# Optimization experiments

Measured on AMD Instinct MI355X. Metric: run time of the kernel, lower is better.

## Reference

```python
import jax, jax.numpy as jnp
import numpy as np

DIM = 512
B = 16
L = 2048
MLP_RATIO = 4
GATE_HID = max(DIM // 4, 8)  # 128
EPS = 1e-5


def _ln(x, g, b):
    mu = jnp.mean(x, axis=-1, keepdims=True)
    var = jnp.mean(jnp.square(x - mu), axis=-1, keepdims=True)
    return (x - mu) * jax.lax.rsqrt(var + EPS) * g + b


def _dwconv(h, w, b, pad):
    # h: [B, C, L], w: [C, 1, k] depthwise
    y = jax.lax.conv_general_dilated(
        h, w, window_strides=(1,), padding=[(pad, pad)],
        dimension_numbers=('NCH', 'OIH', 'NCH'), feature_group_count=h.shape[1])
    return y + b[None, :, None]


def setup_inputs() -> dict:
    key = jax.random.key(0)
    ks = jax.random.split(key, 16)
    d = DIM
    hid = d * MLP_RATIO
    s = lambda k, shape, scale: jax.random.normal(k, shape, dtype=jnp.float32) * scale
    return {
        'x': jax.random.normal(ks[0], (B, L, d), dtype=jnp.float32),
        'ln1_g': jnp.ones((d,), jnp.float32), 'ln1_b': jnp.zeros((d,), jnp.float32),
        'w3': s(ks[1], (d, 1, 3), 0.3), 'b3': jnp.zeros((d,), jnp.float32),
        'w5': s(ks[2], (d, 1, 5), 0.3), 'b5': jnp.zeros((d,), jnp.float32),
        'w7': s(ks[3], (d, 1, 7), 0.3), 'b7': jnp.zeros((d,), jnp.float32),
        'wmix': s(ks[4], (d, d), 0.03), 'bmix': jnp.zeros((d,), jnp.float32),
        'cg_w1': s(ks[5], (d, GATE_HID), 0.03), 'cg_b1': jnp.zeros((GATE_HID,), jnp.float32),
        'cg_w2': s(ks[6], (GATE_HID, d), 0.05), 'cg_b2': jnp.zeros((d,), jnp.float32),
        'wout': s(ks[7], (d, d), 0.03), 'bout': jnp.zeros((d,), jnp.float32),
        'ls1': jnp.full((d,), 1e-4, jnp.float32),
        'ln2_g': jnp.ones((d,), jnp.float32), 'ln2_b': jnp.zeros((d,), jnp.float32),
        'ffn_w1': s(ks[8], (d, hid), 0.03), 'ffn_b1': jnp.zeros((hid,), jnp.float32),
        'ffn_w2': s(ks[9], (hid, d), 0.02), 'ffn_b2': jnp.zeros((d,), jnp.float32),
        'ls2': jnp.full((d,), 1e-4, jnp.float32),
    }


def reference(x, ln1_g, ln1_b, w3, b3, w5, b5, w7, b7, wmix, bmix,
              cg_w1, cg_b1, cg_w2, cg_b2, wout, bout, ls1,
              ln2_g, ln2_b, ffn_w1, ffn_b1, ffn_w2, ffn_b2, ls2):
    gelu = lambda v: jax.nn.gelu(v, approximate=False)
    # norm + transpose to channels-first [B, D, L]
    h = jnp.transpose(_ln(x, ln1_g, ln1_b), (0, 2, 1))
    mixed = (_dwconv(h, w3, b3, 1) + _dwconv(h, w5, b5, 2) + _dwconv(h, w7, b7, 3)) / 3.0
    # 1x1 conv == per-position channel GEMM
    mixed = jnp.einsum('bcl,co->bol', gelu(mixed), wmix.T) + bmix[None, :, None]
    channel_token = jnp.mean(mixed, axis=-1)  # [B, D]
    gate = jax.nn.sigmoid(gelu(channel_token @ cg_w1 + cg_b1) @ cg_w2 + cg_b2)  # [B, D]
    attn_like = jnp.transpose(mixed * gate[:, :, None], (0, 2, 1))  # [B, L, D]
    x = x + (attn_like @ wout + bout) * ls1  # dropout is identity in eval
    h2 = _ln(x, ln2_g, ln2_b)
    x = x + (gelu(h2 @ ffn_w1 + ffn_b1) @ ffn_w2 + ffn_b2) * ls2
    return x
```

## Files before the change

kernel.cpp:

```cpp
#include <hip/hip_runtime.h>
#include <hip/hip_bf16.h>
#include <stdint.h>
#include <math.h>

#define DIMC 512
#define SEQ  2048
#define NB   16
#define MTOT (NB * SEQ)
#define HID  2048

#define SWZ(row) (((row) & 7) << 4)

typedef float v4f __attribute__((ext_vector_type(4)));

__device__ __forceinline__ float bf2f(unsigned short u) {
  union { unsigned int i; float f; } v; v.i = ((unsigned int)u) << 16; return v.f;
}
__device__ __forceinline__ unsigned short f2bf(float f) {
  union { float f; unsigned int i; } v; v.f = f;
  unsigned int r = v.i + 0x7fffu + ((v.i >> 16) & 1u);
  return (unsigned short)(r >> 16);
}
__device__ __forceinline__ float gelu_f(float v) {
  return 0.5f * v * (1.f + erff(v * 0.70710678118654752440f));
}
__device__ __forceinline__ unsigned short pk_fp8(float a, float b) {
  return (unsigned short)__builtin_amdgcn_cvt_pk_fp8_f32(a, b, 0, false);
}
__device__ __forceinline__ unsigned int pk_fp8x4(float a, float b, float c, float d) {
  int lo = __builtin_amdgcn_cvt_pk_fp8_f32(a, b, 0, false);
  return (unsigned int)__builtin_amdgcn_cvt_pk_fp8_f32(c, d, lo, true);
}

typedef __attribute__((address_space(1))) const void cglobal_void;
typedef __attribute__((address_space(3))) void lds_void;
__device__ __forceinline__ void load16_lds(const void* g, void* l) {
  __builtin_amdgcn_global_load_lds((cglobal_void*)g, (lds_void*)l, 16, 0, 0);
}

__global__ __launch_bounds__(256) void pack_w(const float* __restrict__ in,
                                              unsigned char* __restrict__ out,
                                              int R, int C, int trans) {
  int i = blockIdx.x * 256 + threadIdx.x;
  if (i * 2 >= R * C) return;
  int r = (i * 2) / C, c = (i * 2) - r * C;
  float v0, v1;
  if (trans) { v0 = in[(size_t)c * R + r]; v1 = in[(size_t)(c + 1) * R + r]; }
  else       { v0 = in[(size_t)r * C + c]; v1 = in[(size_t)r * C + c + 1]; }
  *(unsigned short*)(out + (size_t)r * C + (c ^ SWZ(r))) = pk_fp8(v0, v1);
}

__global__ __launch_bounds__(256) void ln1_conv(
    const float* __restrict__ x, const float* __restrict__ lg, const float* __restrict__ lb,
    const float* __restrict__ w3, const float* __restrict__ b3,
    const float* __restrict__ w5, const float* __restrict__ b5,
    const float* __restrict__ w7, const float* __restrict__ b7,
    unsigned char* __restrict__ gout, float* __restrict__ gsum) {
  __shared__ __align__(16) unsigned short ht[38 * DIMC];
  int blk = blockIdx.x;
  int b = blk >> 6;
  int l0 = (blk & 63) << 5;
  int tid = threadIdx.x, lane = tid & 63, w = tid >> 6;

  for (int r = w; r < 38; r += 4) {
    int l = l0 - 3 + r;
    unsigned short* hrow = ht + r * DIMC;
    if (l < 0 || l >= SEQ) {
      ushort4 z; z.x = z.y = z.z = z.w = 0;
      *(ushort4*)&hrow[lane * 4] = z;
      *(ushort4*)&hrow[256 + lane * 4] = z;
    } else {
      const float4* xp = (const float4*)(x + ((size_t)(b * SEQ + l)) * DIMC);
      float4 v0 = xp[lane], v1 = xp[lane + 64];
      float s = v0.x + v0.y + v0.z + v0.w + v1.x + v1.y + v1.z + v1.w;
      float q = v0.x * v0.x + v0.y * v0.y + v0.z * v0.z + v0.w * v0.w +
                v1.x * v1.x + v1.y * v1.y + v1.z * v1.z + v1.w * v1.w;
#pragma unroll
      for (int o = 32; o > 0; o >>= 1) { s += __shfl_xor(s, o); q += __shfl_xor(q, o); }
      float mu = s * (1.f / 512.f);
      float rs = rsqrtf(q * (1.f / 512.f) - mu * mu + 1e-5f);
      float4 ga = ((const float4*)lg)[lane], gb = ((const float4*)lg)[lane + 64];
      float4 ba = ((const float4*)lb)[lane], bb = ((const float4*)lb)[lane + 64];
      ushort4 o0, o1;
      o0.x = f2bf((v0.x - mu) * rs * ga.x + ba.x);
      o0.y = f2bf((v0.y - mu) * rs * ga.y + ba.y);
      o0.z = f2bf((v0.z - mu) * rs * ga.z + ba.z);
      o0.w = f2bf((v0.w - mu) * rs * ga.w + ba.w);
      o1.x = f2bf((v1.x - mu) * rs * gb.x + bb.x);
      o1.y = f2bf((v1.y - mu) * rs * gb.y + bb.y);
      o1.z = f2bf((v1.z - mu) * rs * gb.z + bb.z);
      o1.w = f2bf((v1.w - mu) * rs * gb.w + bb.w);
      *(ushort4*)&hrow[lane * 4] = o0;
      *(ushort4*)&hrow[256 + lane * 4] = o1;
    }
  }
  __syncthreads();

  int d0 = tid << 1;
  float t3[2][3], t5[2][5], t7[2][7], cb[2];
#pragma unroll
  for (int j = 0; j < 2; j++) {
    int d = d0 + j;
    cb[j] = b3[d] + b5[d] + b7[d];
#pragma unroll
    for (int t = 0; t < 3; t++) t3[j][t] = w3[d * 3 + t];
#pragma unroll
    for (int t = 0; t < 5; t++) t5[j][t] = w5[d * 5 + t];
#pragma unroll
    for (int t = 0; t < 7; t++) t7[j][t] = w7[d * 7 + t];
  }
  float sum0 = 0.f, sum1 = 0.f;
  size_t rbase = ((size_t)(b * SEQ + l0)) * DIMC;
  for (int l = 0; l < 32; l++) {
    float h0[7], h1[7];
#pragma unroll
    for (int r = 0; r < 7; r++) {
      unsigned int pk = *(const unsigned int*)&ht[(l + r) * DIMC + d0];
      h0[r] = bf2f((unsigned short)pk);
      h1[r] = bf2f((unsigned short)(pk >> 16));
    }
    float a0 = cb[0], a1 = cb[1];
#pragma unroll
    for (int t = 0; t < 7; t++) { a0 += t7[0][t] * h0[t];     a1 += t7[1][t] * h1[t]; }
#pragma unroll
    for (int t = 0; t < 5; t++) { a0 += t5[0][t] * h0[t + 1]; a1 += t5[1][t] * h1[t + 1]; }
#pragma unroll
    for (int t = 0; t < 3; t++) { a0 += t3[0][t] * h0[t + 2]; a1 += t3[1][t] * h1[t + 2]; }
    a0 *= (1.f / 3.f); a1 *= (1.f / 3.f);
    float g0 = gelu_f(a0), g1 = gelu_f(a1);
    *(unsigned short*)(gout + rbase + (size_t)l * DIMC + (d0 ^ SWZ(l))) = pk_fp8(g0, g1);
    sum0 += g0; sum1 += g1;
  }
  atomicAdd(&gsum[b * DIMC + d0], sum0);
  atomicAdd(&gsum[b * DIMC + d0 + 1], sum1);
}

__global__ __launch_bounds__(1024) void gate_kernel(
    const float* __restrict__ gsum, const float* __restrict__ wmix, const float* __restrict__ bmix,
    const float* __restrict__ cg_w1, const float* __restrict__ cg_b1,
    const float* __restrict__ cg_w2, const float* __restrict__ cg_b2,
    float* __restrict__ gate) {
  __shared__ float gbar[512];
  __shared__ float ct[512];
  __shared__ float part2[8][128];
  __shared__ float t1[128];
  __shared__ float part3[2][512];
  int b = blockIdx.x, tid = threadIdx.x;
  int lane = tid & 63, w = tid >> 6;

  if (tid < 512) gbar[tid] = gsum[b * 512 + tid] * (1.f / (float)SEQ);
  __syncthreads();

  {
    const float4* gb4 = (const float4*)gbar;
    float4 g0 = gb4[lane * 2], g1 = gb4[lane * 2 + 1];
#pragma unroll 4
    for (int i = 0; i < 32; i++) {
      int o = w * 32 + i;
      const float4* wr = (const float4*)(wmix + (size_t)o * 512);
      float4 a0 = wr[lane * 2], a1 = wr[lane * 2 + 1];
      float s = a0.x * g0.x + a0.y * g0.y + a0.z * g0.z + a0.w * g0.w +
                a1.x * g1.x + a1.y * g1.y + a1.z * g1.z + a1.w * g1.w;
#pragma unroll
      for (int off = 32; off > 0; off >>= 1) s += __shfl_xor(s, off);
      if (lane == 0) ct[o] = s + bmix[o];
    }
  }
  __syncthreads();

  {
    int h = tid & 127, g = tid >> 7;
    float s = 0.f;
    const float* wp = cg_w1 + (size_t)(g * 64) * 128 + h;
#pragma unroll 8
    for (int c = 0; c < 64; c++) s += ct[g * 64 + c] * wp[c * 128];
    part2[g][h] = s;
  }
  __syncthreads();
  if (tid < 128) {
    float s = cg_b1[tid];
#pragma unroll
    for (int g = 0; g < 8; g++) s += part2[g][tid];
    t1[tid] = gelu_f(s);
  }
  __syncthreads();

  {
    int o = tid & 511, g = tid >> 9;
    float s = 0.f;
    const float* wp = cg_w2 + (size_t)(g * 64) * 512 + o;
#pragma unroll 8
    for (int h = 0; h < 64; h++) s += t1[g * 64 + h] * wp[h * 512];
    part3[g][o] = s;
  }
  __syncthreads();
  if (tid < 512) {
    float s = cg_b2[tid] + part3[0][tid] + part3[1][tid];
    gate[b * 512 + tid] = 1.f / (1.f + expf(-s));
  }
}

__global__ __launch_bounds__(256) void ln2_kernel(
    const float* __restrict__ y, const float* __restrict__ lg, const float* __restrict__ lb,
    unsigned char* __restrict__ h2) {
  int tok = (blockIdx.x << 2) + (threadIdx.x >> 6);
  int lane = threadIdx.x & 63;
  const float4* yp = (const float4*)(y + ((size_t)tok) * DIMC);
  float4 v0 = yp[lane], v1 = yp[lane + 64];
  float s = v0.x + v0.y + v0.z + v0.w + v1.x + v1.y + v1.z + v1.w;
  float q = v0.x * v0.x + v0.y * v0.y + v0.z * v0.z + v0.w * v0.w +
            v1.x * v1.x + v1.y * v1.y + v1.z * v1.z + v1.w * v1.w;
#pragma unroll
  for (int o = 32; o > 0; o >>= 1) { s += __shfl_xor(s, o); q += __shfl_xor(q, o); }
  float mu = s * (1.f / 512.f);
  float rs = rsqrtf(q * (1.f / 512.f) - mu * mu + 1e-5f);
  float4 ga = ((const float4*)lg)[lane], gb = ((const float4*)lg)[lane + 64];
  float4 ba = ((const float4*)lb)[lane], bb = ((const float4*)lb)[lane + 64];
  unsigned char* hp = h2 + (size_t)tok * DIMC;
  int sw = SWZ(tok);
  *(unsigned int*)(hp + ((lane * 4) ^ sw)) = pk_fp8x4(
      (v0.x - mu) * rs * ga.x + ba.x, (v0.y - mu) * rs * ga.y + ba.y,
      (v0.z - mu) * rs * ga.z + ba.z, (v0.w - mu) * rs * ga.w + ba.w);
  *(unsigned int*)(hp + (256 + ((lane * 4) ^ sw))) = pk_fp8x4(
      (v1.x - mu) * rs * gb.x + bb.x, (v1.y - mu) * rs * gb.y + bb.y,
      (v1.z - mu) * rs * gb.z + bb.z, (v1.w - mu) * rs * gb.w + bb.w);
}

template <int MODE>
__global__ __launch_bounds__(256) void gemm_bt(
    const unsigned char* __restrict__ A, int lda,
    const unsigned char* __restrict__ B, int ldb,
    const float* __restrict__ bias, const float* __restrict__ scale,
    const float* __restrict__ resid, void* __restrict__ outp,
    int N, int K, const float* __restrict__ gate) {
  __shared__ __align__(16) unsigned char smem[32768];
  unsigned char* As = smem;
  unsigned char* Bs = smem + 16384;
  float* ebuf = (float*)smem;

  const int m0 = blockIdx.x * 128, n0 = blockIdx.y * 128;
  const int tid = threadIdx.x, lane = tid & 63, w = tid >> 6;
  const int wm = w >> 1, wn = w & 1, quad = lane >> 4, cn = lane & 15;
  const int srow = lane >> 3;
  const int scol = (lane & 7) << 4;
  const int rswz = SWZ(cn);

  v4f acc[4][4];
  v4f zero4 = {0.f, 0.f, 0.f, 0.f};
#pragma unroll
  for (int i = 0; i < 4; i++)
#pragma unroll
    for (int j = 0; j < 4; j++) acc[i][j] = zero4;

  for (int k0 = 0; k0 < K; k0 += 128) {
    __syncthreads();
#pragma unroll
    for (int s = 0; s < 4; s++) {
      int seg = (w << 2) + s;
      int row = (seg << 3) + srow;
      load16_lds(A + (size_t)(m0 + row) * lda + k0 + scol, &As[seg * 1024]);
      load16_lds(B + (size_t)(n0 + row) * ldb + k0 + scol, &Bs[seg * 1024]);
    }
    __syncthreads();
#pragma unroll
    for (int kk = 0; kk < 4; kk++) {
      long af[4], bf[4];
      int pcol = ((kk << 5) + (quad << 3)) ^ rswz;
#pragma unroll
      for (int mt = 0; mt < 4; mt++)
        af[mt] = *(const long*)&As[(wm * 64 + mt * 16 + cn) * 128 + pcol];
#pragma unroll
      for (int nt = 0; nt < 4; nt++)
        bf[nt] = *(const long*)&Bs[(wn * 64 + nt * 16 + cn) * 128 + pcol];
#pragma unroll
      for (int mt = 0; mt < 4; mt++)
#pragma unroll
        for (int nt = 0; nt < 4; nt++)
          acc[mt][nt] = __builtin_amdgcn_mfma_f32_16x16x32_fp8_fp8(af[mt], bf[nt], acc[mt][nt], 0, 0, 0);
    }
  }

  const int bb = (MODE == 1) ? (m0 >> 11) : 0;
#pragma unroll
  for (int h = 0; h < 2; h++) {
    __syncthreads();
    if (wm == h) {
#pragma unroll
      for (int mt = 0; mt < 4; mt++)
#pragma unroll
        for (int nt = 0; nt < 4; nt++)
#pragma unroll
          for (int r = 0; r < 4; r++)
            ebuf[(mt * 16 + quad * 4 + r) * 128 + wn * 64 + nt * 16 + cn] = acc[mt][nt][r];
    }
    __syncthreads();
#pragma unroll
    for (int i = 0; i < 8; i++) {
      int fi = (i << 8) + tid;
      int r = fi >> 5, c4 = fi & 31;
      int row = m0 + (h << 6) + r;
      int col = n0 + (c4 << 2);
      const float* e = &ebuf[fi << 2];
      float v0 = e[0], v1 = e[1], v2 = e[2], v3 = e[3];
      float4 bv = *(const float4*)&bias[col];
      v0 += bv.x; v1 += bv.y; v2 += bv.z; v3 += bv.w;
      size_t idx = (size_t)row * N + col;
      size_t sidx = (size_t)row * N + (col ^ SWZ(row));
      if (MODE == 1) {
        float4 gv = *(const float4*)&gate[bb * 512 + col];
        *(unsigned int*)((unsigned char*)outp + sidx) =
            pk_fp8x4(v0 * gv.x, v1 * gv.y, v2 * gv.z, v3 * gv.w);
      } else if (MODE == 2) {
        float4 sv = *(const float4*)&scale[col];
        float4 rv = *(const float4*)&resid[idx];
        float4 o; o.x = rv.x + v0 * sv.x; o.y = rv.y + v1 * sv.y;
        o.z = rv.z + v2 * sv.z; o.w = rv.w + v3 * sv.w;
        *(float4*)((float*)outp + idx) = o;
      } else if (MODE == 3) {
        *(unsigned int*)((unsigned char*)outp + sidx) =
            pk_fp8x4(gelu_f(v0), gelu_f(v1), gelu_f(v2), gelu_f(v3));
      } else {
        float4 sv = *(const float4*)&scale[col];
        float* op = (float*)outp + idx;
        float4 ov = *(float4*)op;
        float4 o; o.x = ov.x + v0 * sv.x; o.y = ov.y + v1 * sv.y;
        o.z = ov.z + v2 * sv.z; o.w = ov.w + v3 * sv.w;
        *(float4*)op = o;
      }
    }
  }
}

extern "C" void kernel_launch(void* const* d_in, const int* in_sizes, int n_in,
                              void* d_out, int out_size, void* d_ws, size_t ws_size,
                              hipStream_t stream) {
  (void)in_sizes; (void)n_in; (void)out_size; (void)ws_size;
  const float* x     = (const float*)d_in[0];
  const float* ln1_g = (const float*)d_in[1];
  const float* ln1_b = (const float*)d_in[2];
  const float* w3    = (const float*)d_in[3];
  const float* b3    = (const float*)d_in[4];
  const float* w5    = (const float*)d_in[5];
  const float* b5    = (const float*)d_in[6];
  const float* w7    = (const float*)d_in[7];
  const float* b7    = (const float*)d_in[8];
  const float* wmix  = (const float*)d_in[9];
  const float* bmix  = (const float*)d_in[10];
  const float* cg_w1 = (const float*)d_in[11];
  const float* cg_b1 = (const float*)d_in[12];
  const float* cg_w2 = (const float*)d_in[13];
  const float* cg_b2 = (const float*)d_in[14];
  const float* wout  = (const float*)d_in[15];
  const float* bout  = (const float*)d_in[16];
  const float* ls1   = (const float*)d_in[17];
  const float* ln2_g = (const float*)d_in[18];
  const float* ln2_b = (const float*)d_in[19];
  const float* ffn_w1= (const float*)d_in[20];
  const float* ffn_b1= (const float*)d_in[21];
  const float* ffn_w2= (const float*)d_in[22];
  const float* ffn_b2= (const float*)d_in[23];
  const float* ls2   = (const float*)d_in[24];

  char* ws = (char*)d_ws;
  unsigned char* wmix8 = (unsigned char*)(ws + 0);
  unsigned char* wout8 = (unsigned char*)(ws + 262144);
  unsigned char* w18   = (unsigned char*)(ws + 524288);
  unsigned char* w28   = (unsigned char*)(ws + 1572864);
  float*         gsum  = (float*)(ws + 2621440);
  float*         gate  = (float*)(ws + 2654208);
  unsigned char* gbuf  = (unsigned char*)(ws + 3145728);
  unsigned char* attn  = (unsigned char*)(ws + 19922944);
  unsigned char* h2buf = (unsigned char*)(ws + 36700160);
  unsigned char* tbuf  = gbuf;

  hipMemsetAsync(gsum, 0, NB * DIMC * sizeof(float), stream);

  pack_w<<<(512 * 512 / 2 + 255) / 256, 256, 0, stream>>>(wmix,   wmix8, 512, 512, 0);
  pack_w<<<(512 * 512 / 2 + 255) / 256, 256, 0, stream>>>(wout,   wout8, 512, 512, 1);
  pack_w<<<(2048 * 512 / 2 + 255) / 256, 256, 0, stream>>>(ffn_w1, w18, 2048, 512, 1);
  pack_w<<<(2048 * 512 / 2 + 255) / 256, 256, 0, stream>>>(ffn_w2, w28,  512, 2048, 1);

  ln1_conv<<<NB * 64, 256, 0, stream>>>(x, ln1_g, ln1_b, w3, b3, w5, b5, w7, b7, gbuf, gsum);
  gate_kernel<<<NB, 1024, 0, stream>>>(gsum, wmix, bmix, cg_w1, cg_b1, cg_w2, cg_b2, gate);

  dim3 grid_d(MTOT / 128, DIMC / 128);
  gemm_bt<1><<<grid_d, 256, 0, stream>>>(gbuf, 512, wmix8, 512,
                                         bmix, nullptr, nullptr, attn, 512, 512, gate);
  gemm_bt<2><<<grid_d, 256, 0, stream>>>(attn, 512, wout8, 512,
                                         bout, ls1, x, d_out, 512, 512, nullptr);
  ln2_kernel<<<MTOT / 4, 256, 0, stream>>>((const float*)d_out, ln2_g, ln2_b, h2buf);

  const int MC = 16384;
  for (int c = 0; c < 2; c++) {
    size_t r0 = (size_t)c * MC;
    dim3 g3(MC / 128, HID / 128);
    gemm_bt<3><<<g3, 256, 0, stream>>>(h2buf + r0 * 512, 512, w18, 512,
                                       ffn_b1, nullptr, nullptr, tbuf, HID, 512, nullptr);
    dim3 g4(MC / 128, DIMC / 128);
    gemm_bt<4><<<g4, 256, 0, stream>>>(tbuf, 2048, w28, 2048,
                                       ffn_b2, ls2, nullptr,
                                       (float*)d_out + r0 * 512, 512, 2048, nullptr);
  }
}
```

Before: 512.9 us.

## Merge weight packing kernels, use tanh-approx GELU, swizzle epilogue LDS buffer

```diff
diff --git a/kernel.cpp b/kernel.cpp
--- a/kernel.cpp
+++ b/kernel.cpp
@@ -24,6 +24,10 @@
 __device__ __forceinline__ float gelu_f(float v) {
   return 0.5f * v * (1.f + erff(v * 0.70710678118654752440f));
 }
+__device__ __forceinline__ float gelu_fast(float v) {
+  float u2 = 2.f * v * (0.7978845608f + 0.0356774081f * v * v);
+  return v / (1.f + __expf(-u2));
+}
 __device__ __forceinline__ unsigned short pk_fp8(float a, float b) {
   return (unsigned short)__builtin_amdgcn_cvt_pk_fp8_f32(a, b, 0, false);
 }
@@ -38,12 +42,21 @@
   __builtin_amdgcn_global_load_lds((cglobal_void*)g, (lds_void*)l, 16, 0, 0);
 }
 
-__global__ __launch_bounds__(256) void pack_w(const float* __restrict__ in,
-                                              unsigned char* __restrict__ out,
-                                              int R, int C, int trans) {
-  int i = blockIdx.x * 256 + threadIdx.x;
-  if (i * 2 >= R * C) return;
-  int r = (i * 2) / C, c = (i * 2) - r * C;
+__global__ __launch_bounds__(256) void pack_all(
+    const float* __restrict__ wmix, const float* __restrict__ wout,
+    const float* __restrict__ ffn_w1, const float* __restrict__ ffn_w2,
+    unsigned char* __restrict__ wmix8, unsigned char* __restrict__ wout8,
+    unsigned char* __restrict__ w18, unsigned char* __restrict__ w28,
+    float* __restrict__ gsum) {
+  int p = blockIdx.x * 256 + threadIdx.x;
+  if (p < NB * DIMC) gsum[p] = 0.f;
+
+  const float* in; unsigned char* out; int R, C, trans;
+  if (p < 131072)      { in = wmix;   out = wmix8; R = 512;  C = 512;  trans = 0; }
+  else if (p < 262144) { in = wout;   out = wout8; R = 512;  C = 512;  trans = 1; p -= 131072; }
+  else if (p < 786432) { in = ffn_w1; out = w18;   R = 2048; C = 512;  trans = 1; p -= 262144; }
+  else                 { in = ffn_w2; out = w28;   R = 512;  C = 2048; trans = 1; p -= 786432; }
+  int r = (p * 2) / C, c = (p * 2) - r * C;
   float v0, v1;
   if (trans) { v0 = in[(size_t)c * R + r]; v1 = in[(size_t)(c + 1) * R + r]; }
   else       { v0 = in[(size_t)r * C + c]; v1 = in[(size_t)r * C + c + 1]; }
@@ -127,7 +140,7 @@
 #pragma unroll
     for (int t = 0; t < 3; t++) { a0 += t3[0][t] * h0[t + 2]; a1 += t3[1][t] * h1[t + 2]; }
     a0 *= (1.f / 3.f); a1 *= (1.f / 3.f);
-    float g0 = gelu_f(a0), g1 = gelu_f(a1);
+    float g0 = gelu_fast(a0), g1 = gelu_fast(a1);
     *(unsigned short*)(gout + rbase + (size_t)l * DIMC + (d0 ^ SWZ(l))) = pk_fp8(g0, g1);
     sum0 += g0; sum1 += g1;
   }
@@ -285,13 +298,14 @@
   for (int h = 0; h < 2; h++) {
     __syncthreads();
     if (wm == h) {
+      const int exsw = (quad & 1) << 4;
 #pragma unroll
       for (int mt = 0; mt < 4; mt++)
 #pragma unroll
         for (int nt = 0; nt < 4; nt++)
 #pragma unroll
           for (int r = 0; r < 4; r++)
-            ebuf[(mt * 16 + quad * 4 + r) * 128 + wn * 64 + nt * 16 + cn] = acc[mt][nt][r];
+            ebuf[(mt * 16 + quad * 4 + r) * 128 + ((wn * 64 + nt * 16 + cn) ^ exsw)] = acc[mt][nt][r];
     }
     __syncthreads();
 #pragma unroll
@@ -300,7 +314,7 @@
       int r = fi >> 5, c4 = fi & 31;
       int row = m0 + (h << 6) + r;
       int col = n0 + (c4 << 2);
-      const float* e = &ebuf[fi << 2];
+      const float* e = &ebuf[(fi << 2) ^ ((r & 4) << 2)];
       float v0 = e[0], v1 = e[1], v2 = e[2], v3 = e[3];
       float4 bv = *(const float4*)&bias[col];
       v0 += bv.x; v1 += bv.y; v2 += bv.z; v3 += bv.w;
@@ -318,7 +332,7 @@
         *(float4*)((float*)outp + idx) = o;
       } else if (MODE == 3) {
         *(unsigned int*)((unsigned char*)outp + sidx) =
-            pk_fp8x4(gelu_f(v0), gelu_f(v1), gelu_f(v2), gelu_f(v3));
+            pk_fp8x4(gelu_fast(v0), gelu_fast(v1), gelu_fast(v2), gelu_fast(v3));
       } else {
         float4 sv = *(const float4*)&scale[col];
         float* op = (float*)outp + idx;
@@ -373,12 +387,8 @@
   unsigned char* h2buf = (unsigned char*)(ws + 36700160);
   unsigned char* tbuf  = gbuf;
 
-  hipMemsetAsync(gsum, 0, NB * DIMC * sizeof(float), stream);
-
-  pack_w<<<(512 * 512 / 2 + 255) / 256, 256, 0, stream>>>(wmix,   wmix8, 512, 512, 0);
-  pack_w<<<(512 * 512 / 2 + 255) / 256, 256, 0, stream>>>(wout,   wout8, 512, 512, 1);
-  pack_w<<<(2048 * 512 / 2 + 255) / 256, 256, 0, stream>>>(ffn_w1, w18, 2048, 512, 1);
-  pack_w<<<(2048 * 512 / 2 + 255) / 256, 256, 0, stream>>>(ffn_w2, w28,  512, 2048, 1);
+  pack_all<<<1310720 / 256, 256, 0, stream>>>(wmix, wout, ffn_w1, ffn_w2,
+                                              wmix8, wout8, w18, w28, gsum);
 
   ln1_conv<<<NB * 64, 256, 0, stream>>>(x, ln1_g, ln1_b, w3, b3, w5, b5, w7, b7, gbuf, gsum);
   gate_kernel<<<NB, 1024, 0, stream>>>(gsum, wmix, bmix, cg_w1, cg_b1, cg_w2, cg_b2, gate);
```

Measured after the change: 464.4 us. -9.5%, faster.
